# Optimization experiments

Measured on AMD Instinct MI355X. Metric: run time of the kernel, lower is better.

## Reference

```python
import jax, jax.numpy as jnp
import numpy as np

N_NODES = 100000
N_EDGES = 1600000
IN_DIM = 128
HID = 64


def setup_inputs() -> dict:
    key = jax.random.key(0)
    ks = jax.random.split(key, 12)
    s = 1.0 / np.sqrt(IN_DIM)
    sh = 1.0 / np.sqrt(HID)
    return {
        "x": jax.random.normal(ks[0], (N_NODES, IN_DIM), jnp.float32),
        "edge_index": jax.random.randint(ks[1], (2, N_EDGES), 0, N_NODES, jnp.int64)
        if jax.config.jax_enable_x64 else jax.random.randint(ks[1], (2, N_EDGES), 0, N_NODES, jnp.int32),
        "edge_attr": jax.random.uniform(ks[2], (N_EDGES, 1), jnp.float32),
        "Wi": jax.random.normal(ks[3], (IN_DIM, HID), jnp.float32) * s,
        "bi": jnp.zeros((HID,), jnp.float32),
        "W1": jax.random.normal(ks[4], (HID, HID), jnp.float32) * sh,
        "b1": jnp.zeros((HID,), jnp.float32),
        "W2": jax.random.normal(ks[5], (HID, HID), jnp.float32) * sh,
        "b2": jnp.zeros((HID,), jnp.float32),
        "W3": jax.random.normal(ks[6], (HID, HID), jnp.float32) * sh,
        "b3": jnp.zeros((HID,), jnp.float32),
    }


def reference(x, edge_index, edge_attr, Wi, bi, W1, b1, W2, b2, W3, b3):
    src = edge_index[0]
    tgt = edge_index[1]
    w = edge_attr[:, 0:1]  # [E,1]
    h = jax.nn.relu(x @ Wi + bi)  # [N,H]
    states = [h]
    for W, b in ((W1, b1), (W2, b2), (W3, b3)):
        # per-edge weighted message, scatter-add into target nodes
        msgs = jax.ops.segment_sum(h[src] * w, tgt, num_segments=h.shape[0])
        h = jax.nn.relu((h + msgs) @ W + b)
        states.append(h)
    return jnp.stack(states)  # [4, N, H] (list of states in the original)
```

## Files before the change

### kernel.cpp

```cpp
#include <hip/hip_runtime.h>
#include <hip/hip_bf16.h>

#define N_NODES 100000
#define N_EDGES 1600000
#define IN_DIM  128
#define HID     64
#define BIN_NODES 256
#define NBINS   ((N_NODES + BIN_NODES - 1) / BIN_NODES)
#define EB      2048

#define PITCH_IN  152
#define PITCH_HID 88

typedef __attribute__((ext_vector_type(8))) short bf16x8;
typedef __attribute__((ext_vector_type(4))) float f32x4;

__device__ inline unsigned short f2bf(float f) {
    __hip_bfloat16 b = __float2bfloat16(f);
    return *reinterpret_cast<unsigned short*>(&b);
}

__global__ void wf_prep_kernel(const float* __restrict__ Wi,
                               const float* __restrict__ W1,
                               const float* __restrict__ W2,
                               const float* __restrict__ W3,
                               unsigned short* __restrict__ wf_in,
                               unsigned short* __restrict__ wf_hid) {
    int t = blockIdx.x * 256 + threadIdx.x;
    if (t < 8192) {
        int j = t & 7, n16 = (t >> 3) & 15, quad = (t >> 7) & 3, nt = (t >> 9) & 3, kc = t >> 11;
        int k = kc * 32 + quad * 8 + j, n = nt * 16 + n16;
        wf_in[t] = f2bf(Wi[k * HID + n]);
    }
    if (t < 4096) {
        int j = t & 7, n16 = (t >> 3) & 15, quad = (t >> 7) & 3, nt = (t >> 9) & 3, kc = t >> 11;
        int k = kc * 32 + quad * 8 + j, n = nt * 16 + n16;
        wf_hid[t]        = f2bf(W1[k * HID + n]);
        wf_hid[4096 + t] = f2bf(W2[k * HID + n]);
        wf_hid[8192 + t] = f2bf(W3[k * HID + n]);
    }
}

__global__ __launch_bounds__(256) void gemm_in_kernel(
        const float* __restrict__ x,
        const unsigned short* __restrict__ wf,
        const float* __restrict__ bi,
        float* __restrict__ h0,
        __hip_bfloat16* __restrict__ hbf) {
    __shared__ unsigned short sX[64 * PITCH_IN];
    const int tid  = threadIdx.x;
    const int row0 = blockIdx.x * 64;

    #pragma unroll
    for (int it = 0; it < 8; ++it) {
        int i  = tid + it * 256;
        int r  = i >> 5;
        int kq = i & 31;
        int rg = row0 + r;
        float4 v = (rg < N_NODES)
                 ? ((const float4*)x)[(size_t)rg * (IN_DIM / 4) + kq]
                 : make_float4(0.f, 0.f, 0.f, 0.f);
        ushort4 pk;
        pk.x = f2bf(v.x); pk.y = f2bf(v.y); pk.z = f2bf(v.z); pk.w = f2bf(v.w);
        *(ushort4*)(sX + r * PITCH_IN + kq * 4) = pk;
    }
    __syncthreads();

    const int lane = tid & 63;
    const int wid  = tid >> 6;
    const int l16  = lane & 15;
    const int q    = lane >> 4;

    f32x4 acc[4] = {{0,0,0,0},{0,0,0,0},{0,0,0,0},{0,0,0,0}};
    const bf16x8* wf8 = (const bf16x8*)wf;

    #pragma unroll
    for (int kc = 0; kc < 4; ++kc) {
        bf16x8 af = *(const bf16x8*)(sX + (wid * 16 + l16) * PITCH_IN + kc * 32 + q * 8);
        #pragma unroll
        for (int nt = 0; nt < 4; ++nt) {
            bf16x8 bfr = wf8[((kc * 4 + nt) * 4 + q) * 16 + l16];
            acc[nt] = __builtin_amdgcn_mfma_f32_16x16x32_bf16(af, bfr, acc[nt], 0, 0, 0);
        }
    }

    #pragma unroll
    for (int nt = 0; nt < 4; ++nt) {
        float bb = bi[nt * 16 + l16];
        #pragma unroll
        for (int reg = 0; reg < 4; ++reg) {
            int rg = row0 + wid * 16 + q * 4 + reg;
            if (rg < N_NODES) {
                float v = fmaxf(acc[nt][reg] + bb, 0.0f);
                h0 [(size_t)rg * HID + nt * 16 + l16] = v;
                hbf[(size_t)rg * HID + nt * 16 + l16] = __float2bfloat16(v);
            }
        }
    }
}

__global__ void bin_hist_kernel(const int* __restrict__ tgt,
                                int* __restrict__ g_bin_cnt) {
    __shared__ int cnt[NBINS];
    for (int i = threadIdx.x; i < NBINS; i += 256) cnt[i] = 0;
    __syncthreads();
    const int e0 = blockIdx.x * EB;
    for (int i = threadIdx.x; i < EB; i += 256) {
        int e = e0 + i;
        if (e < N_EDGES) atomicAdd(&cnt[tgt[e] >> 8], 1);
    }
    __syncthreads();
    for (int i = threadIdx.x; i < NBINS; i += 256)
        if (cnt[i]) atomicAdd(&g_bin_cnt[i], cnt[i]);
}

__global__ void bin_scan_kernel(const int* __restrict__ g_bin_cnt,
                                int* __restrict__ g_bin_offs,
                                int* __restrict__ g_bin_cursor) {
    __shared__ int s[512];
    const int tid = threadIdx.x;
    int v = (tid < NBINS) ? g_bin_cnt[tid] : 0;
    s[tid] = v;
    __syncthreads();
    for (int off = 1; off < 512; off <<= 1) {
        int t = (tid >= off) ? s[tid - off] : 0;
        __syncthreads();
        s[tid] += t;
        __syncthreads();
    }
    if (tid < NBINS) { g_bin_offs[tid] = s[tid] - v; g_bin_cursor[tid] = s[tid] - v; }
}

__global__ void bin_scatter_kernel(const int* __restrict__ src,
                                   const int* __restrict__ tgt,
                                   const float* __restrict__ ea,
                                   int* __restrict__ g_bin_cursor,
                                   unsigned long long* __restrict__ binned) {
    __shared__ int cnt[NBINS];
    __shared__ int base[NBINS];
    __shared__ int cur[NBINS];
    for (int i = threadIdx.x; i < NBINS; i += 256) cnt[i] = 0;
    __syncthreads();

    const int e0 = blockIdx.x * EB;
    int myb[EB / 256];
    unsigned long long myrec[EB / 256];
    #pragma unroll
    for (int i = 0; i < EB / 256; ++i) {
        int e = e0 + threadIdx.x + i * 256;
        if (e < N_EDGES) {
            int t = tgt[e];
            int b = t >> 8;
            myb[i] = b;
            myrec[i] = ((unsigned long long)(unsigned)__float_as_int(ea[e]) << 32)
                     | ((unsigned)(t & 255) << 17) | (unsigned)src[e];
            atomicAdd(&cnt[b], 1);
        } else {
            myb[i] = -1;
        }
    }
    __syncthreads();
    for (int i = threadIdx.x; i < NBINS; i += 256) {
        cur[i]  = 0;
        base[i] = cnt[i] ? atomicAdd(&g_bin_cursor[i], cnt[i]) : 0;
    }
    __syncthreads();
    #pragma unroll
    for (int i = 0; i < EB / 256; ++i) {
        if (myb[i] >= 0) {
            int r = atomicAdd(&cur[myb[i]], 1);
            binned[base[myb[i]] + r] = myrec[i];
        }
    }
}

__global__ void fine_fill_kernel(const unsigned long long* __restrict__ binned,
                                 const int* __restrict__ g_bin_offs,
                                 const int* __restrict__ g_bin_cnt,
                                 int* __restrict__ offs,
                                 int* __restrict__ counts,
                                 unsigned long long* __restrict__ pairs) {
    __shared__ int ncnt[256];
    __shared__ int nbase[256];
    __shared__ int wsum[4];
    const int b    = blockIdx.x;
    const int tid  = threadIdx.x;
    const int ebeg = g_bin_offs[b];
    const int ecnt = g_bin_cnt[b];

    ncnt[tid] = 0;
    __syncthreads();
    for (int i = tid; i < ecnt; i += 256) {
        int lt = (int)((binned[ebeg + i] >> 17) & 255);
        atomicAdd(&ncnt[lt], 1);
    }
    __syncthreads();

    const int lane = tid & 63, wid = tid >> 6;
    int v  = ncnt[tid];
    int sc = v;
    #pragma unroll
    for (int d = 1; d < 64; d <<= 1) {
        int t = __shfl_up(sc, d);
        if (lane >= d) sc += t;
    }
    if (lane == 63) wsum[wid] = sc;
    __syncthreads();
    int wb = 0;
    for (int w = 0; w < wid; ++w) wb += wsum[w];
    int excl = wb + sc - v;
    nbase[tid] = excl;

    const int node = b * BIN_NODES + tid;
    if (node < N_NODES) { offs[node] = ebeg + excl; counts[node] = v; }

    ncnt[tid] = 0;
    __syncthreads();
    for (int i = tid; i < ecnt; i += 256) {
        unsigned long long rec = binned[ebeg + i];
        int lt = (int)((rec >> 17) & 255);
        int r  = atomicAdd(&ncnt[lt], 1);
        pairs[ebeg + nbase[lt] + r] =
            (rec & 0xFFFFFFFF00000000ull) | (rec & 0x1FFFFull);
    }
}

__global__ __launch_bounds__(256) void agg_gemm_kernel(
        const float* __restrict__ h,
        const __hip_bfloat16* __restrict__ hbf_in,
        const int* __restrict__ offs,
        const int* __restrict__ counts,
        const int2* __restrict__ pairs,
        const unsigned short* __restrict__ wf,
        const float* __restrict__ b,
        float* __restrict__ hnext,
        __hip_bfloat16* __restrict__ hbf_out) {
    __shared__ unsigned short sX[64 * PITCH_HID];
    const int tid  = threadIdx.x;
    const int row0 = blockIdx.x * 64;
    const int lane = tid & 63;
    const int wid  = tid >> 6;
    const int grp  = lane >> 4;
    const int sub  = lane & 15;

    for (int t = 0; t < 16; ++t) {
        const int node = row0 + wid * 16 + t;
        if (node < N_NODES) {
            const int beg = offs[node];
            const int cnt = counts[node];
            float ax = 0.f, ay = 0.f, az = 0.f, aw = 0.f;
            if (cnt > 0) {
                const int last = cnt - 1;
                for (int i = 0; i < cnt; i += 8) {
                    int e0 = i + grp;
                    int e1 = i + 4 + grp;
                    bool l0 = (e0 <= last);
                    bool l1 = (e1 <= last);
                    int2 p0 = pairs[beg + (l0 ? e0 : last)];
                    int2 p1 = pairs[beg + (l1 ? e1 : last)];
                    uint2 g0 = *(const uint2*)(hbf_in + (size_t)p0.x * HID + sub * 4);
                    uint2 g1 = *(const uint2*)(hbf_in + (size_t)p1.x * HID + sub * 4);
                    float w0 = l0 ? __int_as_float(p0.y) : 0.0f;
                    float w1 = l1 ? __int_as_float(p1.y) : 0.0f;
                    ax += w0 * __uint_as_float(g0.x << 16);
                    ay += w0 * __uint_as_float(g0.x & 0xFFFF0000u);
                    az += w0 * __uint_as_float(g0.y << 16);
                    aw += w0 * __uint_as_float(g0.y & 0xFFFF0000u);
                    ax += w1 * __uint_as_float(g1.x << 16);
                    ay += w1 * __uint_as_float(g1.x & 0xFFFF0000u);
                    az += w1 * __uint_as_float(g1.y << 16);
                    aw += w1 * __uint_as_float(g1.y & 0xFFFF0000u);
                }
            }
            ax += __shfl_xor(ax, 16); ay += __shfl_xor(ay, 16);
            az += __shfl_xor(az, 16); aw += __shfl_xor(aw, 16);
            ax += __shfl_xor(ax, 32); ay += __shfl_xor(ay, 32);
            az += __shfl_xor(az, 32); aw += __shfl_xor(aw, 32);
            if (grp == 0) {
                const float4 hv = *(const float4*)(h + (size_t)node * HID + sub * 4);
                ushort4 pk;
                pk.x = f2bf(hv.x + ax); pk.y = f2bf(hv.y + ay);
                pk.z = f2bf(hv.z + az); pk.w = f2bf(hv.w + aw);
                *(ushort4*)(sX + (wid * 16 + t) * PITCH_HID + sub * 4) = pk;
            }
        } else if (grp == 0) {
            ushort4 z; z.x = 0; z.y = 0; z.z = 0; z.w = 0;
            *(ushort4*)(sX + (wid * 16 + t) * PITCH_HID + sub * 4) = z;
        }
    }
    __syncthreads();

    const int l16 = lane & 15;
    const int q   = lane >> 4;

    f32x4 acc[4] = {{0,0,0,0},{0,0,0,0},{0,0,0,0},{0,0,0,0}};
    const bf16x8* wf8 = (const bf16x8*)wf;

    #pragma unroll
    for (int kc = 0; kc < 2; ++kc) {
        bf16x8 af = *(const bf16x8*)(sX + (wid * 16 + l16) * PITCH_HID + kc * 32 + q * 8);
        #pragma unroll
        for (int nt = 0; nt < 4; ++nt) {
            bf16x8 bfr = wf8[((kc * 4 + nt) * 4 + q) * 16 + l16];
            acc[nt] = __builtin_amdgcn_mfma_f32_16x16x32_bf16(af, bfr, acc[nt], 0, 0, 0);
        }
    }

    #pragma unroll
    for (int nt = 0; nt < 4; ++nt) {
        float bb = b[nt * 16 + l16];
        #pragma unroll
        for (int reg = 0; reg < 4; ++reg) {
            int rg = row0 + wid * 16 + q * 4 + reg;
            if (rg < N_NODES) {
                float v = fmaxf(acc[nt][reg] + bb, 0.0f);
                hnext  [(size_t)rg * HID + nt * 16 + l16] = v;
                hbf_out[(size_t)rg * HID + nt * 16 + l16] = __float2bfloat16(v);
            }
        }
    }
}

extern "C" void kernel_launch(void* const* d_in, const int* in_sizes, int n_in,
                              void* d_out, int out_size, void* d_ws, size_t ws_size,
                              hipStream_t stream) {
    const float* x   = (const float*)d_in[0];
    const int*   ei  = (const int*)  d_in[1];
    const float* ea  = (const float*)d_in[2];
    const float* Wi  = (const float*)d_in[3];
    const float* bi  = (const float*)d_in[4];
    const float* W1  = (const float*)d_in[5];
    const float* b1  = (const float*)d_in[6];
    const float* W2  = (const float*)d_in[7];
    const float* b2  = (const float*)d_in[8];
    const float* W3  = (const float*)d_in[9];
    const float* b3  = (const float*)d_in[10];
    const float* bl[3] = { b1, b2, b3 };
    float* out = (float*)d_out;

    const int* src = ei;
    const int* tgt = ei + N_EDGES;

    unsigned long long* binned = (unsigned long long*)d_ws;
    int* offs         = (int*)(binned + N_EDGES);
    int* counts       = offs + N_NODES;
    int* g_bin_cnt    = counts + N_NODES;
    int* g_bin_offs   = g_bin_cnt + NBINS;
    int* g_bin_cursor = g_bin_offs + NBINS;
    int* pad          = g_bin_cursor + NBINS;
    unsigned long long* pairs = (unsigned long long*)(pad + 1);
    __hip_bfloat16* hbf0 = (__hip_bfloat16*)(pairs + N_EDGES);
    __hip_bfloat16* hbf1 = hbf0 + (size_t)N_NODES * HID;
    unsigned short* wf_in  = (unsigned short*)(hbf1 + (size_t)N_NODES * HID);
    unsigned short* wf_hid = wf_in + 8192;

    hipMemsetAsync(g_bin_cnt, 0, NBINS * sizeof(int), stream);

    wf_prep_kernel<<<32, 256, 0, stream>>>(Wi, W1, W2, W3, wf_in, wf_hid);

    const int eb_blocks = (N_EDGES + EB - 1) / EB;
    bin_hist_kernel   <<<eb_blocks, 256, 0, stream>>>(tgt, g_bin_cnt);
    bin_scan_kernel   <<<1, 512, 0, stream>>>(g_bin_cnt, g_bin_offs, g_bin_cursor);
    bin_scatter_kernel<<<eb_blocks, 256, 0, stream>>>(src, tgt, ea, g_bin_cursor, binned);
    fine_fill_kernel  <<<NBINS, 256, 0, stream>>>(binned, g_bin_offs, g_bin_cnt,
                                                  offs, counts, pairs);

    const int gemm_blocks = (N_NODES + 63) / 64;
    gemm_in_kernel<<<gemm_blocks, 256, 0, stream>>>(x, wf_in, bi, out, hbf0);

    __hip_bfloat16* hin  = hbf0;
    __hip_bfloat16* hout = hbf1;
    for (int l = 0; l < 3; ++l) {
        const float* hl = out + (size_t)l * N_NODES * HID;
        float* hn       = out + (size_t)(l + 1) * N_NODES * HID;
        agg_gemm_kernel<<<gemm_blocks, 256, 0, stream>>>(
            hl, hin, offs, counts, (const int2*)pairs,
            wf_hid + (size_t)l * 4096, bl[l], hn, hout);
        __hip_bfloat16* t = hin; hin = hout; hout = t;
    }
}
```

Before: 453.5 us.

## Widen fine_fill blocks, unroll gather, preload offsets, skip last bf16 store

fine_fill_kernel now runs 1024 threads per bin, with the scan restricted to the first 256 threads. agg_gemm preloads per-node offsets and counts once per wave and broadcasts them by shuffle. It issues the self-state load early and unrolls the edge gather to four outstanding loads per lane. The final layer skips writing the unused bf16 copy. The goal is more memory-level parallelism in the gather and less redundant traffic, at the cost of higher register pressure and __syncthreads calls placed in divergent branches.

Result: slower. 479.8 us (+5.8%).

```diff
diff --git a/kernel.cpp b/kernel.cpp
--- a/kernel.cpp
+++ b/kernel.cpp
@@ -174,7 +174,8 @@
     }
 }
 
-__global__ void fine_fill_kernel(const unsigned long long* __restrict__ binned,
+__global__ __launch_bounds__(1024) void fine_fill_kernel(
+                                 const unsigned long long* __restrict__ binned,
                                  const int* __restrict__ g_bin_offs,
                                  const int* __restrict__ g_bin_cnt,
                                  int* __restrict__ offs,
@@ -188,35 +189,39 @@
     const int ebeg = g_bin_offs[b];
     const int ecnt = g_bin_cnt[b];
 
-    ncnt[tid] = 0;
-    __syncthreads();
-    for (int i = tid; i < ecnt; i += 256) {
+    if (tid < 256) ncnt[tid] = 0;
+    __syncthreads();
+    for (int i = tid; i < ecnt; i += 1024) {
         int lt = (int)((binned[ebeg + i] >> 17) & 255);
         atomicAdd(&ncnt[lt], 1);
     }
     __syncthreads();
 
-    const int lane = tid & 63, wid = tid >> 6;
-    int v  = ncnt[tid];
-    int sc = v;
-    #pragma unroll
-    for (int d = 1; d < 64; d <<= 1) {
-        int t = __shfl_up(sc, d);
-        if (lane >= d) sc += t;
-    }
-    if (lane == 63) wsum[wid] = sc;
-    __syncthreads();
-    int wb = 0;
-    for (int w = 0; w < wid; ++w) wb += wsum[w];
-    int excl = wb + sc - v;
-    nbase[tid] = excl;
-
-    const int node = b * BIN_NODES + tid;
-    if (node < N_NODES) { offs[node] = ebeg + excl; counts[node] = v; }
-
-    ncnt[tid] = 0;
-    __syncthreads();
-    for (int i = tid; i < ecnt; i += 256) {
+    if (tid < 256) {
+        const int lane = tid & 63, wid = tid >> 6;
+        int v  = ncnt[tid];
+        int sc = v;
+        #pragma unroll
+        for (int d = 1; d < 64; d <<= 1) {
+            int t = __shfl_up(sc, d);
+            if (lane >= d) sc += t;
+        }
+        if (lane == 63) wsum[wid] = sc;
+        __syncthreads();
+        int wb = 0;
+        for (int w = 0; w < wid; ++w) wb += wsum[w];
+        int excl = wb + sc - v;
+        nbase[tid] = excl;
+
+        const int node = b * BIN_NODES + tid;
+        if (node < N_NODES) { offs[node] = ebeg + excl; counts[node] = v; }
+
+        ncnt[tid] = 0;
+    } else {
+        __syncthreads();
+    }
+    __syncthreads();
+    for (int i = tid; i < ecnt; i += 1024) {
         unsigned long long rec = binned[ebeg + i];
         int lt = (int)((rec >> 17) & 255);
         int r  = atomicAdd(&ncnt[lt], 1);
@@ -234,7 +239,8 @@
         const unsigned short* __restrict__ wf,
         const float* __restrict__ b,
         float* __restrict__ hnext,
-        __hip_bfloat16* __restrict__ hbf_out) {
+        __hip_bfloat16* __restrict__ hbf_out,
+        const int store_bf) {
     __shared__ unsigned short sX[64 * PITCH_HID];
     const int tid  = threadIdx.x;
     const int row0 = blockIdx.x * 64;
@@ -243,25 +249,43 @@
     const int grp  = lane >> 4;
     const int sub  = lane & 15;
 
+    int offv = 0, cntv = 0;
+    {
+        int nl = row0 + wid * 16 + (lane & 15);
+        if (lane < 16 && nl < N_NODES) { offv = offs[nl]; cntv = counts[nl]; }
+    }
+
     for (int t = 0; t < 16; ++t) {
         const int node = row0 + wid * 16 + t;
         if (node < N_NODES) {
-            const int beg = offs[node];
-            const int cnt = counts[node];
+            const int beg = __shfl(offv, t);
+            const int cnt = __shfl(cntv, t);
+            float4 hv;
+            if (grp == 0) hv = *(const float4*)(h + (size_t)node * HID + sub * 4);
             float ax = 0.f, ay = 0.f, az = 0.f, aw = 0.f;
             if (cnt > 0) {
                 const int last = cnt - 1;
-                for (int i = 0; i < cnt; i += 8) {
+                for (int i = 0; i < cnt; i += 16) {
                     int e0 = i + grp;
                     int e1 = i + 4 + grp;
+                    int e2 = i + 8 + grp;
+                    int e3 = i + 12 + grp;
                     bool l0 = (e0 <= last);
                     bool l1 = (e1 <= last);
+                    bool l2 = (e2 <= last);
+                    bool l3 = (e3 <= last);
                     int2 p0 = pairs[beg + (l0 ? e0 : last)];
                     int2 p1 = pairs[beg + (l1 ? e1 : last)];
+                    int2 p2 = pairs[beg + (l2 ? e2 : last)];
+                    int2 p3 = pairs[beg + (l3 ? e3 : last)];
                     uint2 g0 = *(const uint2*)(hbf_in + (size_t)p0.x * HID + sub * 4);
                     uint2 g1 = *(const uint2*)(hbf_in + (size_t)p1.x * HID + sub * 4);
+                    uint2 g2 = *(const uint2*)(hbf_in + (size_t)p2.x * HID + sub * 4);
+                    uint2 g3 = *(const uint2*)(hbf_in + (size_t)p3.x * HID + sub * 4);
                     float w0 = l0 ? __int_as_float(p0.y) : 0.0f;
                     float w1 = l1 ? __int_as_float(p1.y) : 0.0f;
+                    float w2 = l2 ? __int_as_float(p2.y) : 0.0f;
+                    float w3 = l3 ? __int_as_float(p3.y) : 0.0f;
                     ax += w0 * __uint_as_float(g0.x << 16);
                     ay += w0 * __uint_as_float(g0.x & 0xFFFF0000u);
                     az += w0 * __uint_as_float(g0.y << 16);
@@ -270,6 +294,14 @@
                     ay += w1 * __uint_as_float(g1.x & 0xFFFF0000u);
                     az += w1 * __uint_as_float(g1.y << 16);
                     aw += w1 * __uint_as_float(g1.y & 0xFFFF0000u);
+                    ax += w2 * __uint_as_float(g2.x << 16);
+                    ay += w2 * __uint_as_float(g2.x & 0xFFFF0000u);
+                    az += w2 * __uint_as_float(g2.y << 16);
+                    aw += w2 * __uint_as_float(g2.y & 0xFFFF0000u);
+                    ax += w3 * __uint_as_float(g3.x << 16);
+                    ay += w3 * __uint_as_float(g3.x & 0xFFFF0000u);
+                    az += w3 * __uint_as_float(g3.y << 16);
+                    aw += w3 * __uint_as_float(g3.y & 0xFFFF0000u);
                 }
             }
             ax += __shfl_xor(ax, 16); ay += __shfl_xor(ay, 16);
@@ -277,7 +309,6 @@
             ax += __shfl_xor(ax, 32); ay += __shfl_xor(ay, 32);
             az += __shfl_xor(az, 32); aw += __shfl_xor(aw, 32);
             if (grp == 0) {
-                const float4 hv = *(const float4*)(h + (size_t)node * HID + sub * 4);
                 ushort4 pk;
                 pk.x = f2bf(hv.x + ax); pk.y = f2bf(hv.y + ay);
                 pk.z = f2bf(hv.z + az); pk.w = f2bf(hv.w + aw);
@@ -314,8 +345,9 @@
             int rg = row0 + wid * 16 + q * 4 + reg;
             if (rg < N_NODES) {
                 float v = fmaxf(acc[nt][reg] + bb, 0.0f);
-                hnext  [(size_t)rg * HID + nt * 16 + l16] = v;
-                hbf_out[(size_t)rg * HID + nt * 16 + l16] = __float2bfloat16(v);
+                hnext[(size_t)rg * HID + nt * 16 + l16] = v;
+                if (store_bf)
+                    hbf_out[(size_t)rg * HID + nt * 16 + l16] = __float2bfloat16(v);
             }
         }
     }
@@ -362,8 +394,8 @@
     bin_hist_kernel   <<<eb_blocks, 256, 0, stream>>>(tgt, g_bin_cnt);
     bin_scan_kernel   <<<1, 512, 0, stream>>>(g_bin_cnt, g_bin_offs, g_bin_cursor);
     bin_scatter_kernel<<<eb_blocks, 256, 0, stream>>>(src, tgt, ea, g_bin_cursor, binned);
-    fine_fill_kernel  <<<NBINS, 256, 0, stream>>>(binned, g_bin_offs, g_bin_cnt,
-                                                  offs, counts, pairs);
+    fine_fill_kernel  <<<NBINS, 1024, 0, stream>>>(binned, g_bin_offs, g_bin_cnt,
+                                                   offs, counts, pairs);
 
     const int gemm_blocks = (N_NODES + 63) / 64;
     gemm_in_kernel<<<gemm_blocks, 256, 0, stream>>>(x, wf_in, bi, out, hbf0);
@@ -375,7 +407,7 @@
         float* hn       = out + (size_t)(l + 1) * N_NODES * HID;
         agg_gemm_kernel<<<gemm_blocks, 256, 0, stream>>>(
             hl, hin, offs, counts, (const int2*)pairs,
-            wf_hid + (size_t)l * 4096, bl[l], hn, hout);
+            wf_hid + (size_t)l * 4096, bl[l], hn, hout, (l < 2) ? 1 : 0);
         __hip_bfloat16* t = hin; hin = hout; hout = t;
     }
 }
```

## Coalesce edge-pair loads via wave shuffles, widen fine_fill, skip final bf16 store

Applied to the files above, without the earlier changes.

In the aggregation loop, each wave now loads up to 64 edge pairs at once with one coalesced load and hands the source index and weight to lanes through __shfl, so lanes no longer issue a separate pair load per edge. fine_fill_kernel runs with 1024 threads per block to make the binned-edge passes more parallel, with the scan still limited to the first 256 threads. The last layer no longer writes its bf16 copy, which nothing reads. The fine_fill change puts __syncthreads inside divergent branches, which relies on the barriers in both branches matching up.

Result: faster. 441.5 us (-2.7%).

```diff
diff --git a/kernel.cpp b/kernel.cpp
--- a/kernel.cpp
+++ b/kernel.cpp
@@ -174,7 +174,8 @@
     }
 }
 
-__global__ void fine_fill_kernel(const unsigned long long* __restrict__ binned,
+__global__ __launch_bounds__(1024) void fine_fill_kernel(
+                                 const unsigned long long* __restrict__ binned,
                                  const int* __restrict__ g_bin_offs,
                                  const int* __restrict__ g_bin_cnt,
                                  int* __restrict__ offs,
@@ -188,35 +189,39 @@
     const int ebeg = g_bin_offs[b];
     const int ecnt = g_bin_cnt[b];
 
-    ncnt[tid] = 0;
-    __syncthreads();
-    for (int i = tid; i < ecnt; i += 256) {
+    if (tid < 256) ncnt[tid] = 0;
+    __syncthreads();
+    for (int i = tid; i < ecnt; i += 1024) {
         int lt = (int)((binned[ebeg + i] >> 17) & 255);
         atomicAdd(&ncnt[lt], 1);
     }
     __syncthreads();
 
-    const int lane = tid & 63, wid = tid >> 6;
-    int v  = ncnt[tid];
-    int sc = v;
-    #pragma unroll
-    for (int d = 1; d < 64; d <<= 1) {
-        int t = __shfl_up(sc, d);
-        if (lane >= d) sc += t;
-    }
-    if (lane == 63) wsum[wid] = sc;
-    __syncthreads();
-    int wb = 0;
-    for (int w = 0; w < wid; ++w) wb += wsum[w];
-    int excl = wb + sc - v;
-    nbase[tid] = excl;
-
-    const int node = b * BIN_NODES + tid;
-    if (node < N_NODES) { offs[node] = ebeg + excl; counts[node] = v; }
-
-    ncnt[tid] = 0;
-    __syncthreads();
-    for (int i = tid; i < ecnt; i += 256) {
+    if (tid < 256) {
+        const int lane = tid & 63, wid = tid >> 6;
+        int v  = ncnt[tid];
+        int sc = v;
+        #pragma unroll
+        for (int d = 1; d < 64; d <<= 1) {
+            int t = __shfl_up(sc, d);
+            if (lane >= d) sc += t;
+        }
+        if (lane == 63) wsum[wid] = sc;
+        __syncthreads();
+        int wb = 0;
+        for (int w = 0; w < wid; ++w) wb += wsum[w];
+        int excl = wb + sc - v;
+        nbase[tid] = excl;
+
+        const int node = b * BIN_NODES + tid;
+        if (node < N_NODES) { offs[node] = ebeg + excl; counts[node] = v; }
+
+        ncnt[tid] = 0;
+    } else {
+        __syncthreads();
+    }
+    __syncthreads();
+    for (int i = tid; i < ecnt; i += 1024) {
         unsigned long long rec = binned[ebeg + i];
         int lt = (int)((rec >> 17) & 255);
         int r  = atomicAdd(&ncnt[lt], 1);
@@ -234,7 +239,8 @@
         const unsigned short* __restrict__ wf,
         const float* __restrict__ b,
         float* __restrict__ hnext,
-        __hip_bfloat16* __restrict__ hbf_out) {
+        __hip_bfloat16* __restrict__ hbf_out,
+        const int store_bf) {
     __shared__ unsigned short sX[64 * PITCH_HID];
     const int tid  = threadIdx.x;
     const int row0 = blockIdx.x * 64;
@@ -249,19 +255,24 @@
             const int beg = offs[node];
             const int cnt = counts[node];
             float ax = 0.f, ay = 0.f, az = 0.f, aw = 0.f;
-            if (cnt > 0) {
-                const int last = cnt - 1;
-                for (int i = 0; i < cnt; i += 8) {
+            for (int j0 = 0; j0 < cnt; j0 += 64) {
+                int idx = beg + j0 + lane;
+                int2 pl = pairs[min(idx, N_EDGES - 1)];
+                const int nb   = min(64, cnt - j0);
+                const int last = nb - 1;
+                for (int i = 0; i < nb; i += 8) {
                     int e0 = i + grp;
                     int e1 = i + 4 + grp;
                     bool l0 = (e0 <= last);
                     bool l1 = (e1 <= last);
-                    int2 p0 = pairs[beg + (l0 ? e0 : last)];
-                    int2 p1 = pairs[beg + (l1 ? e1 : last)];
-                    uint2 g0 = *(const uint2*)(hbf_in + (size_t)p0.x * HID + sub * 4);
-                    uint2 g1 = *(const uint2*)(hbf_in + (size_t)p1.x * HID + sub * 4);
-                    float w0 = l0 ? __int_as_float(p0.y) : 0.0f;
-                    float w1 = l1 ? __int_as_float(p1.y) : 0.0f;
+                    int s0 = __shfl(pl.x, l0 ? e0 : last);
+                    int w0i = __shfl(pl.y, l0 ? e0 : last);
+                    int s1 = __shfl(pl.x, l1 ? e1 : last);
+                    int w1i = __shfl(pl.y, l1 ? e1 : last);
+                    uint2 g0 = *(const uint2*)(hbf_in + (size_t)s0 * HID + sub * 4);
+                    uint2 g1 = *(const uint2*)(hbf_in + (size_t)s1 * HID + sub * 4);
+                    float w0 = l0 ? __int_as_float(w0i) : 0.0f;
+                    float w1 = l1 ? __int_as_float(w1i) : 0.0f;
                     ax += w0 * __uint_as_float(g0.x << 16);
                     ay += w0 * __uint_as_float(g0.x & 0xFFFF0000u);
                     az += w0 * __uint_as_float(g0.y << 16);
@@ -314,8 +325,9 @@
             int rg = row0 + wid * 16 + q * 4 + reg;
             if (rg < N_NODES) {
                 float v = fmaxf(acc[nt][reg] + bb, 0.0f);
-                hnext  [(size_t)rg * HID + nt * 16 + l16] = v;
-                hbf_out[(size_t)rg * HID + nt * 16 + l16] = __float2bfloat16(v);
+                hnext[(size_t)rg * HID + nt * 16 + l16] = v;
+                if (store_bf)
+                    hbf_out[(size_t)rg * HID + nt * 16 + l16] = __float2bfloat16(v);
             }
         }
     }
@@ -362,8 +374,8 @@
     bin_hist_kernel   <<<eb_blocks, 256, 0, stream>>>(tgt, g_bin_cnt);
     bin_scan_kernel   <<<1, 512, 0, stream>>>(g_bin_cnt, g_bin_offs, g_bin_cursor);
     bin_scatter_kernel<<<eb_blocks, 256, 0, stream>>>(src, tgt, ea, g_bin_cursor, binned);
-    fine_fill_kernel  <<<NBINS, 256, 0, stream>>>(binned, g_bin_offs, g_bin_cnt,
-                                                  offs, counts, pairs);
+    fine_fill_kernel  <<<NBINS, 1024, 0, stream>>>(binned, g_bin_offs, g_bin_cnt,
+                                                   offs, counts, pairs);
 
     const int gemm_blocks = (N_NODES + 63) / 64;
     gemm_in_kernel<<<gemm_blocks, 256, 0, stream>>>(x, wf_in, bi, out, hbf0);
@@ -375,7 +387,7 @@
         float* hn       = out + (size_t)(l + 1) * N_NODES * HID;
         agg_gemm_kernel<<<gemm_blocks, 256, 0, stream>>>(
             hl, hin, offs, counts, (const int2*)pairs,
-            wf_hid + (size_t)l * 4096, bl[l], hn, hout);
+            wf_hid + (size_t)l * 4096, bl[l], hn, hout, (l < 2) ? 1 : 0);
         __hip_bfloat16* t = hin; hin = hout; hout = t;
     }
 }
```
